# Kernel optimization log

Hardware: AMD Instinct MI355X
Metric: run time of the kernel (lower is better)

## Reference

```python
import jax, jax.numpy as jnp
import numpy as np

N_NODES = 50000
N_EDGES = 600000
IN_DIM = 128
OUT_DIM = 128
N_REL = 32
N_BASES = 4
BN_EPS = 1e-5


def setup_inputs() -> dict:
    key = jax.random.key(0)
    ks = jax.random.split(key, 8)
    entity_emb = jax.random.normal(ks[0], (N_NODES, IN_DIM), dtype=jnp.float32)
    bases = jax.random.normal(ks[1], (N_BASES, IN_DIM, OUT_DIM), dtype=jnp.float32) * 0.05
    coefficients = jax.random.normal(ks[2], (N_REL, N_BASES), dtype=jnp.float32) * 0.5
    W_loop = jax.random.normal(ks[3], (IN_DIM, OUT_DIM), dtype=jnp.float32) * 0.05
    b_loop = jnp.zeros((OUT_DIM,), dtype=jnp.float32)
    gamma = jnp.ones((OUT_DIM,), dtype=jnp.float32)
    beta = jnp.zeros((OUT_DIM,), dtype=jnp.float32)
    edge_index = jax.random.randint(ks[4], (2, N_EDGES), 0, N_NODES, dtype=jnp.int32)
    edge_type = jax.random.randint(ks[5], (N_EDGES,), 0, N_REL, dtype=jnp.int32)
    return {"entity_emb": entity_emb, "bases": bases, "coefficients": coefficients,
            "W_loop": W_loop, "b_loop": b_loop, "gamma": gamma, "beta": beta,
            "edge_index": edge_index, "edge_type": edge_type}


def reference(entity_emb, bases, coefficients, W_loop, b_loop, gamma, beta, edge_index, edge_type):
    N = entity_emb.shape[0]
    # self-loop linear
    out = entity_emb @ W_loop + b_loop  # [N, out_dim]
    # basis decomposition: per-relation weight W[r] = sum_b coeff[r,b] * bases[b]
    W = jnp.einsum('rb,bio->rio', coefficients, bases)  # [R, in, out]
    src, dst = edge_index[0], edge_index[1]
    # per-edge message: entity_emb[src_e] @ W[edge_type_e]  (vectorizes the per-relation loop)
    msg = jnp.einsum('ei,eio->eo', entity_emb[src], W[edge_type])  # [E, out]
    out = out + jax.ops.segment_sum(msg, dst, num_segments=N)
    # degree normalization (in-degree over all edges, clamped at 1)
    deg = jax.ops.segment_sum(jnp.ones_like(dst, dtype=out.dtype), dst, num_segments=N)
    out = out / jnp.maximum(deg, 1.0)[:, None]
    # BatchNorm1d (training mode: biased batch stats over node dim)
    mean = jnp.mean(out, axis=0)
    var = jnp.mean((out - mean) ** 2, axis=0)
    out = (out - mean) / jnp.sqrt(var + BN_EPS) * gamma + beta
    return jax.nn.relu(out)
```

## Files before the change

### kernel.cpp

```cpp
#include <hip/hip_runtime.h>
#include <cstdint>

#define NN 50000
#define NE 600000
#define NPAIRS 1563
#define GSTRIDE 512

typedef unsigned short ushort_t;
typedef __bf16 bf16_t;
typedef __attribute__((ext_vector_type(8))) bf16_t bf16x8;
typedef __attribute__((ext_vector_type(8))) ushort_t ushort8;
typedef __attribute__((ext_vector_type(4))) float f32x4;
typedef __attribute__((ext_vector_type(2))) float f32x2;

#define WT_OFF   0ul
#define XGG_OFF  40960ul
#define XBF_OFF  12845056ul
#define CNT_OFF  16046080ul
#define CUR_OFF  16096080ul
#define BSUM_OFF 16146080ul
#define BSCN_OFF 16146208ul
#define CS_OFF   16146336ul
#define CSQ_OFF  16146464ul
#define SDONE_OFF 16146592ul

__device__ __forceinline__ float2 bf2_to_f2(uint32_t u) {
    float2 r;
    r.x = __uint_as_float(u << 16);
    r.y = __uint_as_float(u & 0xffff0000u);
    return r;
}

__device__ __forceinline__ ushort_t f2bf(float f) {
    uint32_t u = __float_as_uint(f);
    u = (u + 0x7fffu + ((u >> 16) & 1u)) >> 16;
    return (ushort_t)u;
}

__device__ __forceinline__ uint32_t f2bf2(float x, float y) {
    return (uint32_t)f2bf(x) | ((uint32_t)f2bf(y) << 16);
}

__device__ __forceinline__ void async_copy16(const void* g, void* l) {
    __builtin_amdgcn_global_load_lds(
        (const __attribute__((address_space(1))) void*)g,
        (__attribute__((address_space(3))) void*)l, 16, 0, 0);
}

__global__ __launch_bounds__(256) void k_pre(
    const float* __restrict__ X, const float* __restrict__ Wl,
    const float* __restrict__ bases, const int* __restrict__ eidx,
    ushort_t* __restrict__ WT, ushort_t* __restrict__ Xbf,
    int* __restrict__ cnt)
{
    const int b = blockIdx.x;
    const int tid = threadIdx.x;
    if (b < 320) {
        const int i = b * 256 + tid;
        const int n = i / 640;
        const int kk = i - n * 640;
        float v;
        if (kk < 128) v = Wl[kk * 128 + n];
        else {
            const int j = kk - 128;
            v = bases[(size_t)(j >> 7) * 16384 + (j & 127) * 128 + n];
        }
        WT[i] = f2bf(v);
    } else if (b < 3445) {
        const int tile = b - 320;
        const int row = tid >> 4, gc = tid & 15;
        const int node = tile * 16 + row;
        const float4* p = (const float4*)(X + (size_t)node * 128 + gc * 8);
        const float4 a = p[0], c = p[1];
        ushort_t t8[8] = { f2bf(a.x), f2bf(a.y), f2bf(a.z), f2bf(a.w),
                           f2bf(c.x), f2bf(c.y), f2bf(c.z), f2bf(c.w) };
        *(uint4*)(Xbf + (size_t)node * 128 + gc * 8) = *(const uint4*)t8;
    } else {
        const int* __restrict__ dst = eidx + NE;
        for (int e = (b - 3445) * 256 + tid; e < NE; e += 2048 * 256)
            atomicAdd(cnt + dst[e], 1);
    }
}

__global__ __launch_bounds__(256) void k_scan12(
    const int* __restrict__ cnt, int* __restrict__ curs,
    int* __restrict__ bsum, int* __restrict__ bscan,
    int* __restrict__ sdone, int nblk)
{
    __shared__ int sh[256];
    __shared__ int lastFlag;
    const int tid = threadIdx.x;
    const int i0 = blockIdx.x * 512 + tid * 2;
    const int v0 = (i0 < NN) ? cnt[i0] : 0;
    const int v1 = (i0 + 1 < NN) ? cnt[i0 + 1] : 0;
    int s = v0 + v1;
    sh[tid] = s;
    __syncthreads();
#pragma unroll
    for (int off = 1; off < 256; off <<= 1) {
        int t = (tid >= off) ? sh[tid - off] : 0;
        __syncthreads();
        sh[tid] += t;
        __syncthreads();
    }
    const int excl = sh[tid] - s;
    if (i0 < NN) curs[i0] = excl;
    if (i0 + 1 < NN) curs[i0 + 1] = excl + v0;
    if (tid == 255) {
        bsum[blockIdx.x] = sh[255];
        __threadfence();
        lastFlag = (atomicAdd(sdone, 1) == (int)gridDim.x - 1);
    }
    __syncthreads();
    if (!lastFlag) return;

    __threadfence();
    const int v = (tid < nblk) ? bsum[tid] : 0;
    __syncthreads();
    sh[tid] = v;
    __syncthreads();
#pragma unroll
    for (int off = 1; off < 256; off <<= 1) {
        int t = (tid >= off) ? sh[tid - off] : 0;
        __syncthreads();
        sh[tid] += t;
        __syncthreads();
    }
    if (tid < nblk) bscan[tid] = sh[tid] - v;
}

__global__ __launch_bounds__(256) void k_scatter(
    const int* __restrict__ eidx, const int* __restrict__ etype,
    int* __restrict__ curs, const int* __restrict__ bscan,
    uint32_t* __restrict__ epack)
{
    const int* __restrict__ src = eidx;
    const int* __restrict__ dst = eidx + NE;
    for (int e = blockIdx.x * 256 + threadIdx.x; e < NE; e += gridDim.x * 256) {
        const int d = dst[e];
        const int pos = atomicAdd(curs + d, 1) + bscan[d >> 9];
        epack[pos] = (uint32_t)src[e] | ((uint32_t)etype[e] << 16);
    }
}

__device__ __forceinline__ void accum_pk(
    const uint4 xv, const float4 cw, f32x2* m2)
{
    f32x2 x2[4];
    float2 p;
    p = bf2_to_f2(xv.x); x2[0] = f32x2{p.x, p.y};
    p = bf2_to_f2(xv.y); x2[1] = f32x2{p.x, p.y};
    p = bf2_to_f2(xv.z); x2[2] = f32x2{p.x, p.y};
    p = bf2_to_f2(xv.w); x2[3] = f32x2{p.x, p.y};
#pragma unroll
    for (int c2 = 0; c2 < 4; ++c2) {
        m2[0 * 4 + c2] += cw.x * x2[c2];
        m2[1 * 4 + c2] += cw.y * x2[c2];
        m2[2 * 4 + c2] += cw.z * x2[c2];
        m2[3 * 4 + c2] += cw.w * x2[c2];
    }
}

__global__ __launch_bounds__(256, 4) void k_gather(
    const ushort_t* __restrict__ Xbf, const uint32_t* __restrict__ epack,
    const int* __restrict__ cnt, const int* __restrict__ curs,
    const int* __restrict__ bscan, const float* __restrict__ coeff,
    ushort_t* __restrict__ XG_G)
{
    const int lane = threadIdx.x & 63;
    const int w = threadIdx.x >> 6;
    const int sub = lane >> 4;
    const int k = lane & 15;
    const int tile = blockIdx.x;
    const int d = tile * 16 + w * 4 + sub;

    const int n = cnt[d];
    const int end = curs[d] + bscan[d >> 9];
    int j = end - n;

    f32x2 m2[16];
#pragma unroll
    for (int i = 0; i < 16; ++i) m2[i] = f32x2{0.f, 0.f};

    for (; j + 7 < end; j += 8) {
        uint32_t ep[8];
#pragma unroll
        for (int i = 0; i < 8; ++i) ep[i] = epack[j + i];
        uint4 xv[8];
        float4 cw[8];
#pragma unroll
        for (int i = 0; i < 8; ++i) {
            const int s = ep[i] & 0xffff;
            const int t = ep[i] >> 16;
            xv[i] = *(const uint4*)(Xbf + (size_t)s * 128 + k * 8);
            cw[i] = *(const float4*)(coeff + t * 4);
        }
#pragma unroll
        for (int i = 0; i < 8; ++i) accum_pk(xv[i], cw[i], m2);
    }
    if (j + 3 < end) {
        uint32_t ep[4];
#pragma unroll
        for (int i = 0; i < 4; ++i) ep[i] = epack[j + i];
        uint4 xv[4];
        float4 cw[4];
#pragma unroll
        for (int i = 0; i < 4; ++i) {
            const int s = ep[i] & 0xffff;
            const int t = ep[i] >> 16;
            xv[i] = *(const uint4*)(Xbf + (size_t)s * 128 + k * 8);
            cw[i] = *(const float4*)(coeff + t * 4);
        }
#pragma unroll
        for (int i = 0; i < 4; ++i) accum_pk(xv[i], cw[i], m2);
        j += 4;
    }
    for (; j < end; ++j) {
        const uint32_t ep = epack[j];
        const int s = ep & 0xffff;
        const int t = ep >> 16;
        const uint4 xv = *(const uint4*)(Xbf + (size_t)s * 128 + k * 8);
        const float4 cw = *(const float4*)(coeff + t * 4);
        accum_pk(xv, cw, m2);
    }

    uint32_t* gb = (uint32_t*)(XG_G + (size_t)tile * 8192);
#pragma unroll
    for (int b = 0; b < 4; ++b) {
        uint4 v;
        v.x = f2bf2(m2[b * 4 + 0][0], m2[b * 4 + 0][1]);
        v.y = f2bf2(m2[b * 4 + 1][0], m2[b * 4 + 1][1]);
        v.z = f2bf2(m2[b * 4 + 2][0], m2[b * 4 + 2][1]);
        v.w = f2bf2(m2[b * 4 + 3][0], m2[b * 4 + 3][1]);
        *(uint4*)(gb + (b * 16 + k) * 64 + (w * 4 + sub) * 4) = v;
    }
}

__global__ __launch_bounds__(256, 2) void k_gemm_f(
    const ushort_t* __restrict__ XG_G, const ushort_t* __restrict__ WT,
    const ushort_t* __restrict__ Xbf, const float* __restrict__ bl,
    const int* __restrict__ cnt, float* __restrict__ out,
    float* __restrict__ colsum, float* __restrict__ colsq)
{
    __shared__ ushort_t As[2][2][10240];
    const int tid = threadIdx.x;
    const int lane = tid & 63;
    const int w = tid >> 6;
    const int m = lane & 15;
    const int quad = lane >> 4;

    auto stage = [&](int buf, int pr) {
#pragma unroll
        for (int j = 0; j < 10; ++j) {
            const int idx = w * 10 + j;
            const int tl = idx / 20;
            const int off = idx - tl * 20;
            const int tile = pr * 2 + tl;
            const ushort_t* src;
            if (off < 4) {
                const int node = tile * 16 + (lane & 15);
                const int g = off * 4 + (lane >> 4);
                src = Xbf + (size_t)node * 128 + g * 8;
            } else {
                src = XG_G + (size_t)tile * 8192 + (off - 4) * 512 + lane * 8;
            }
            async_copy16(src, &As[buf][tl][off * 512]);
        }
    };

    int p = blockIdx.x;
    stage(0, p);

    const ushort_t* bp0 = WT + (size_t)(w * 32 + m) * 640 + quad * 8;
    const ushort_t* bp1 = bp0 + 16 * 640;
    ushort8 B0[20], B1[20];
#pragma unroll
    for (int c = 0; c < 20; ++c) {
        B0[c] = *(const ushort8*)(bp0 + c * 32);
        B1[c] = *(const ushort8*)(bp1 + c * 32);
    }
    const float blv0 = bl[w * 32 + m];
    const float blv1 = bl[w * 32 + 16 + m];
    float s0 = 0.f, q0 = 0.f, s1 = 0.f, q1 = 0.f;

    __syncthreads();

    int buf = 0;
    while (p < NPAIRS) {
        const int pn = p + GSTRIDE;
        if (pn < NPAIRS) stage(buf ^ 1, pn);

        f32x4 cc[2][2];
#pragma unroll
        for (int rt = 0; rt < 2; ++rt)
#pragma unroll
            for (int ct = 0; ct < 2; ++ct)
#pragma unroll
                for (int i = 0; i < 4; ++i) cc[rt][ct][i] = 0.f;

#pragma unroll
        for (int c = 0; c < 20; ++c) {
            const int aoff = (c * 4 + quad) * 128 + m * 8;
            const bf16x8 a0 = __builtin_bit_cast(bf16x8, *(const ushort8*)&As[buf][0][aoff]);
            const bf16x8 a1 = __builtin_bit_cast(bf16x8, *(const ushort8*)&As[buf][1][aoff]);
            const bf16x8 b0 = __builtin_bit_cast(bf16x8, B0[c]);
            const bf16x8 b1 = __builtin_bit_cast(bf16x8, B1[c]);
            cc[0][0] = __builtin_amdgcn_mfma_f32_16x16x32_bf16(a0, b0, cc[0][0], 0, 0, 0);
            cc[0][1] = __builtin_amdgcn_mfma_f32_16x16x32_bf16(a0, b1, cc[0][1], 0, 0, 0);
            cc[1][0] = __builtin_amdgcn_mfma_f32_16x16x32_bf16(a1, b0, cc[1][0], 0, 0, 0);
            cc[1][1] = __builtin_amdgcn_mfma_f32_16x16x32_bf16(a1, b1, cc[1][1], 0, 0, 0);
        }

        const int row0 = p * 32;
#pragma unroll
        for (int rt = 0; rt < 2; ++rt) {
            const int rowb = row0 + rt * 16 + quad * 4;
#pragma unroll
            for (int r = 0; r < 4; ++r) {
                const int row = rowb + r;
                if (row < NN) {
                    const int dg = cnt[row];
                    const float inv = 1.0f / (float)((dg > 0) ? dg : 1);
                    float* po = out + (size_t)row * 128 + w * 32 + m;
                    const float v0 = (cc[rt][0][r] + blv0) * inv;
                    const float v1 = (cc[rt][1][r] + blv1) * inv;
                    po[0]  = v0;
                    po[16] = v1;
                    s0 += v0; q0 += v0 * v0;
                    s1 += v1; q1 += v1 * v1;
                }
            }
        }

        if (pn < NPAIRS) __syncthreads();
        buf ^= 1;
        p = pn;
    }

    s0 += __shfl_down(s0, 32); q0 += __shfl_down(q0, 32);
    s0 += __shfl_down(s0, 16); q0 += __shfl_down(q0, 16);
    s1 += __shfl_down(s1, 32); q1 += __shfl_down(q1, 32);
    s1 += __shfl_down(s1, 16); q1 += __shfl_down(q1, 16);
    if (lane < 16) {
        atomicAdd(colsum + w * 32 + lane, s0);
        atomicAdd(colsq  + w * 32 + lane, q0);
        atomicAdd(colsum + w * 32 + 16 + lane, s1);
        atomicAdd(colsq  + w * 32 + 16 + lane, q1);
    }
}

__global__ __launch_bounds__(256) void k_bn_relu(
    float* __restrict__ out, const float* __restrict__ colsum,
    const float* __restrict__ colsq, const float* __restrict__ gamma,
    const float* __restrict__ beta)
{
    __shared__ float sc[128], sh[128];
    const int tid = threadIdx.x;
    if (tid < 128) {
        const float mean = colsum[tid] * (1.0f / NN);
        const float var = colsq[tid] * (1.0f / NN) - mean * mean;
        const float g = gamma[tid] * rsqrtf(var + 1e-5f);
        sc[tid] = g;
        sh[tid] = beta[tid] - mean * g;
    }
    __syncthreads();
    const int total = NN * 32;
    for (int i = blockIdx.x * 256 + tid; i < total; i += gridDim.x * 256) {
        const int c = (i & 31) << 2;
        float4 v = *(float4*)(out + (size_t)i * 4);
        v.x = fmaxf(fmaf(v.x, sc[c + 0], sh[c + 0]), 0.f);
        v.y = fmaxf(fmaf(v.y, sc[c + 1], sh[c + 1]), 0.f);
        v.z = fmaxf(fmaf(v.z, sc[c + 2], sh[c + 2]), 0.f);
        v.w = fmaxf(fmaf(v.w, sc[c + 3], sh[c + 3]), 0.f);
        *(float4*)(out + (size_t)i * 4) = v;
    }
}

extern "C" void kernel_launch(void* const* d_in, const int* in_sizes, int n_in,
                              void* d_out, int out_size, void* d_ws, size_t ws_size,
                              hipStream_t stream)
{
    const float* X      = (const float*)d_in[0];
    const float* bases  = (const float*)d_in[1];
    const float* coeff  = (const float*)d_in[2];
    const float* Wl     = (const float*)d_in[3];
    const float* bl     = (const float*)d_in[4];
    const float* gamma  = (const float*)d_in[5];
    const float* beta   = (const float*)d_in[6];
    const int*   eidx   = (const int*)d_in[7];
    const int*   etype  = (const int*)d_in[8];
    float* out = (float*)d_out;

    float* ws = (float*)d_ws;
    ushort_t* WT     = (ushort_t*)(ws + WT_OFF);
    ushort_t* XG_G   = (ushort_t*)(ws + XGG_OFF);
    ushort_t* Xbf    = (ushort_t*)(ws + XBF_OFF);
    int*      cnt    = (int*)(ws + CNT_OFF);
    int*      curs   = (int*)(ws + CUR_OFF);
    int*      bsum   = (int*)(ws + BSUM_OFF);
    int*      bscan  = (int*)(ws + BSCN_OFF);
    float*    colsum = ws + CS_OFF;
    float*    colsq  = ws + CSQ_OFF;
    int*      sdone  = (int*)(ws + SDONE_OFF);
    uint32_t* epack  = (uint32_t*)d_out;

    hipMemsetAsync(cnt, 0, (SDONE_OFF + 1 - CNT_OFF) * sizeof(float), stream);

    const int nblk_scan = (NN + 511) / 512;

    k_pre<<<5493, 256, 0, stream>>>(X, Wl, bases, eidx, WT, Xbf, cnt);
    k_scan12<<<nblk_scan, 256, 0, stream>>>(cnt, curs, bsum, bscan, sdone,
                                            nblk_scan);
    k_scatter<<<2048, 256, 0, stream>>>(eidx, etype, curs, bscan, epack);
    k_gather<<<3125, 256, 0, stream>>>(Xbf, epack, cnt, curs, bscan, coeff,
                                       XG_G);
    k_gemm_f<<<GSTRIDE, 256, 0, stream>>>(XG_G, WT, Xbf, bl, cnt,
                                          out, colsum, colsq);
    k_bn_relu<<<1024, 256, 0, stream>>>(out, colsum, colsq, gamma, beta);
}
```

Baseline: 249.0 us.

## Shrink GEMM block tile to 16 rows and stream B from global

The fused GEMM now processes one 16-row tile per iteration instead of a 32-row pair. It uses half the shared memory and drops the 40 register-resident B fragments, loading B directly from global (L1/L2-cached) on every MFMA step. The grid doubles to 1024 blocks and launch bounds allow 4 blocks per SM, trading more B load traffic and less reuse of each B fragment for higher occupancy and better latency hiding. The row bounds check is removed because 3125 tiles of 16 rows cover exactly 50000 rows.

```diff
diff --git a/kernel.cpp b/kernel.cpp
--- a/kernel.cpp
+++ b/kernel.cpp
@@ -3,8 +3,8 @@
 
 #define NN 50000
 #define NE 600000
-#define NPAIRS 1563
-#define GSTRIDE 512
+#define NTILES 3125
+#define GEMM_GRID 1024
 
 typedef unsigned short ushort_t;
 typedef __bf16 bf16_t;
@@ -236,26 +236,23 @@
     }
 }
 
-__global__ __launch_bounds__(256, 2) void k_gemm_f(
+__global__ __launch_bounds__(256, 4) void k_gemm_f(
     const ushort_t* __restrict__ XG_G, const ushort_t* __restrict__ WT,
     const ushort_t* __restrict__ Xbf, const float* __restrict__ bl,
     const int* __restrict__ cnt, float* __restrict__ out,
     float* __restrict__ colsum, float* __restrict__ colsq)
 {
-    __shared__ ushort_t As[2][2][10240];
+    __shared__ ushort_t As[2][10240];
     const int tid = threadIdx.x;
     const int lane = tid & 63;
     const int w = tid >> 6;
     const int m = lane & 15;
     const int quad = lane >> 4;
 
-    auto stage = [&](int buf, int pr) {
-#pragma unroll
-        for (int j = 0; j < 10; ++j) {
-            const int idx = w * 10 + j;
-            const int tl = idx / 20;
-            const int off = idx - tl * 20;
-            const int tile = pr * 2 + tl;
+    auto stage = [&](int buf, int tile) {
+#pragma unroll
+        for (int j = 0; j < 5; ++j) {
+            const int off = w * 5 + j;
             const ushort_t* src;
             if (off < 4) {
                 const int node = tile * 16 + (lane & 15);
@@ -264,21 +261,15 @@
             } else {
                 src = XG_G + (size_t)tile * 8192 + (off - 4) * 512 + lane * 8;
             }
-            async_copy16(src, &As[buf][tl][off * 512]);
+            async_copy16(src, &As[buf][off * 512]);
         }
     };
 
-    int p = blockIdx.x;
-    stage(0, p);
+    int t = blockIdx.x;
+    stage(0, t);
 
     const ushort_t* bp0 = WT + (size_t)(w * 32 + m) * 640 + quad * 8;
     const ushort_t* bp1 = bp0 + 16 * 640;
-    ushort8 B0[20], B1[20];
-#pragma unroll
-    for (int c = 0; c < 20; ++c) {
-        B0[c] = *(const ushort8*)(bp0 + c * 32);
-        B1[c] = *(const ushort8*)(bp1 + c * 32);
-    }
     const float blv0 = bl[w * 32 + m];
     const float blv1 = bl[w * 32 + 16 + m];
     float s0 = 0.f, q0 = 0.f, s1 = 0.f, q1 = 0.f;
@@ -286,55 +277,44 @@
     __syncthreads();
 
     int buf = 0;
-    while (p < NPAIRS) {
-        const int pn = p + GSTRIDE;
-        if (pn < NPAIRS) stage(buf ^ 1, pn);
-
-        f32x4 cc[2][2];
-#pragma unroll
-        for (int rt = 0; rt < 2; ++rt)
-#pragma unroll
-            for (int ct = 0; ct < 2; ++ct)
-#pragma unroll
-                for (int i = 0; i < 4; ++i) cc[rt][ct][i] = 0.f;
+    while (t < NTILES) {
+        const int tn = t + GEMM_GRID;
+        if (tn < NTILES) stage(buf ^ 1, tn);
+
+        f32x4 cc[2];
+#pragma unroll
+        for (int ct = 0; ct < 2; ++ct)
+#pragma unroll
+            for (int i = 0; i < 4; ++i) cc[ct][i] = 0.f;
 
 #pragma unroll
         for (int c = 0; c < 20; ++c) {
             const int aoff = (c * 4 + quad) * 128 + m * 8;
-            const bf16x8 a0 = __builtin_bit_cast(bf16x8, *(const ushort8*)&As[buf][0][aoff]);
-            const bf16x8 a1 = __builtin_bit_cast(bf16x8, *(const ushort8*)&As[buf][1][aoff]);
-            const bf16x8 b0 = __builtin_bit_cast(bf16x8, B0[c]);
-            const bf16x8 b1 = __builtin_bit_cast(bf16x8, B1[c]);
-            cc[0][0] = __builtin_amdgcn_mfma_f32_16x16x32_bf16(a0, b0, cc[0][0], 0, 0, 0);
-            cc[0][1] = __builtin_amdgcn_mfma_f32_16x16x32_bf16(a0, b1, cc[0][1], 0, 0, 0);
-            cc[1][0] = __builtin_amdgcn_mfma_f32_16x16x32_bf16(a1, b0, cc[1][0], 0, 0, 0);
-            cc[1][1] = __builtin_amdgcn_mfma_f32_16x16x32_bf16(a1, b1, cc[1][1], 0, 0, 0);
-        }
-
-        const int row0 = p * 32;
-#pragma unroll
-        for (int rt = 0; rt < 2; ++rt) {
-            const int rowb = row0 + rt * 16 + quad * 4;
-#pragma unroll
-            for (int r = 0; r < 4; ++r) {
-                const int row = rowb + r;
-                if (row < NN) {
-                    const int dg = cnt[row];
-                    const float inv = 1.0f / (float)((dg > 0) ? dg : 1);
-                    float* po = out + (size_t)row * 128 + w * 32 + m;
-                    const float v0 = (cc[rt][0][r] + blv0) * inv;
-                    const float v1 = (cc[rt][1][r] + blv1) * inv;
-                    po[0]  = v0;
-                    po[16] = v1;
-                    s0 += v0; q0 += v0 * v0;
-                    s1 += v1; q1 += v1 * v1;
-                }
-            }
-        }
-
-        if (pn < NPAIRS) __syncthreads();
+            const bf16x8 a  = __builtin_bit_cast(bf16x8, *(const ushort8*)&As[buf][aoff]);
+            const bf16x8 b0 = __builtin_bit_cast(bf16x8, *(const ushort8*)(bp0 + c * 32));
+            const bf16x8 b1 = __builtin_bit_cast(bf16x8, *(const ushort8*)(bp1 + c * 32));
+            cc[0] = __builtin_amdgcn_mfma_f32_16x16x32_bf16(a, b0, cc[0], 0, 0, 0);
+            cc[1] = __builtin_amdgcn_mfma_f32_16x16x32_bf16(a, b1, cc[1], 0, 0, 0);
+        }
+
+        const int rowb = t * 16 + quad * 4;
+#pragma unroll
+        for (int r = 0; r < 4; ++r) {
+            const int row = rowb + r;
+            const int dg = cnt[row];
+            const float inv = 1.0f / (float)((dg > 0) ? dg : 1);
+            float* po = out + (size_t)row * 128 + w * 32 + m;
+            const float v0 = (cc[0][r] + blv0) * inv;
+            const float v1 = (cc[1][r] + blv1) * inv;
+            po[0]  = v0;
+            po[16] = v1;
+            s0 += v0; q0 += v0 * v0;
+            s1 += v1; q1 += v1 * v1;
+        }
+
+        if (tn < NTILES) __syncthreads();
         buf ^= 1;
-        p = pn;
+        t = tn;
     }
 
     s0 += __shfl_down(s0, 32); q0 += __shfl_down(q0, 32);
@@ -414,7 +394,7 @@
     k_scatter<<<2048, 256, 0, stream>>>(eidx, etype, curs, bscan, epack);
     k_gather<<<3125, 256, 0, stream>>>(Xbf, epack, cnt, curs, bscan, coeff,
                                        XG_G);
-    k_gemm_f<<<GSTRIDE, 256, 0, stream>>>(XG_G, WT, Xbf, bl, cnt,
-                                          out, colsum, colsq);
+    k_gemm_f<<<GEMM_GRID, 256, 0, stream>>>(XG_G, WT, Xbf, bl, cnt,
+                                            out, colsum, colsq);
     k_bn_relu<<<1024, 256, 0, stream>>>(out, colsum, colsq, gamma, beta);
 }
```

New measurement: 296.1 us. 1.19x slower.
